# Optimization experiments

Measured on AMD Instinct MI355X. Metric: run time of the kernel, lower is better.

## Reference

```python
import jax, jax.numpy as jnp
import numpy as np

SEQ_LEN = 4096
D_MODEL = 1024
NUM_POLES = 64


def setup_inputs() -> dict:
    key = jax.random.key(0)
    k1, k2, k3 = jax.random.split(key, 3)
    z = jax.random.normal(k1, (SEQ_LEN,), dtype=jnp.float32)
    poles = jax.random.normal(k2, (D_MODEL, NUM_POLES), dtype=jnp.float32) * 0.1
    residues = jax.random.normal(k3, (D_MODEL, NUM_POLES), dtype=jnp.float32) * 0.01
    return {"z": z, "poles": poles, "residues": residues}


def reference(z, poles, residues):
    # z: (S,), poles/residues: (D, P) -> out: (S, D)
    # Cauchy sum: out[s, d] = sum_p residues[d, p] / (z[s] - poles[d, p])
    denom = z[:, None, None] - poles[None, :, :]          # (S, D, P)
    result = jnp.sum(residues[None, :, :] / denom, axis=-1)  # (S, D)
    return result
```

## Files before the change

kernel.cpp:

```cpp
#include <hip/hip_runtime.h>
#include <hip/hip_bf16.h>

#define S_TOTAL 4096
#define D_TOTAL 1024
#define NPOLES  64
#define NPAIRS  32
#define S_PER_BLOCK 32
#define BLOCK 256

__device__ __forceinline__ float sanitize_finite(float x) {
    const float lim = 1.0e38f;
    const unsigned u = __float_as_uint(x);
    if ((u & 0x7f800000u) == 0x7f800000u)
        return (u & 0x80000000u) ? -lim : lim;
    return fminf(fmaxf(x, -lim), lim);
}

__global__ __launch_bounds__(BLOCK, 2) void cauchy_pair_kernel(
    const float* __restrict__ z,
    const float* __restrict__ poles,
    const float* __restrict__ residues,
    float* __restrict__ out)
{
    const int d  = blockIdx.y * BLOCK + threadIdx.x;
    const int s0 = blockIdx.x * S_PER_BLOCK;

    float cA[NPAIRS], cB[NPAIRS], cS[NPAIRS], cP[NPAIRS];
    const float* pp = poles    + (size_t)d * NPOLES;
    const float* rr = residues + (size_t)d * NPOLES;
#pragma unroll
    for (int i = 0; i < NPOLES / 4; ++i) {
        const float4 p4 = *reinterpret_cast<const float4*>(pp + 4 * i);
        const float4 r4 = *reinterpret_cast<const float4*>(rr + 4 * i);
        const int q = 2 * i;
        cS[q + 0] = p4.x + p4.y;
        cP[q + 0] = p4.x * p4.y;
        cA[q + 0] = r4.x + r4.y;
        cB[q + 0] = -fmaf(r4.x, p4.y, r4.y * p4.x);
        cS[q + 1] = p4.z + p4.w;
        cP[q + 1] = p4.z * p4.w;
        cA[q + 1] = r4.z + r4.w;
        cB[q + 1] = -fmaf(r4.z, p4.w, r4.w * p4.z);
    }

    for (int si = 0; si < S_PER_BLOCK; si += 4) {
        const float z0 = z[s0 + si + 0];
        const float z1 = z[s0 + si + 1];
        const float z2 = z[s0 + si + 2];
        const float z3 = z[s0 + si + 3];
        float a0 = 0.f, a1 = 0.f, a2 = 0.f, a3 = 0.f;
#pragma unroll
        for (int q = 0; q < NPAIRS; ++q) {
            const float A = cA[q], B = cB[q], S = cS[q], P = cP[q];
            {   const float den = fmaf(z0, z0 - S, P);
                a0 = fmaf(fmaf(A, z0, B), __builtin_amdgcn_rcpf(den), a0); }
            {   const float den = fmaf(z1, z1 - S, P);
                a1 = fmaf(fmaf(A, z1, B), __builtin_amdgcn_rcpf(den), a1); }
            {   const float den = fmaf(z2, z2 - S, P);
                a2 = fmaf(fmaf(A, z2, B), __builtin_amdgcn_rcpf(den), a2); }
            {   const float den = fmaf(z3, z3 - S, P);
                a3 = fmaf(fmaf(A, z3, B), __builtin_amdgcn_rcpf(den), a3); }
        }
        out[(size_t)(s0 + si + 0) * D_TOTAL + d] = sanitize_finite(a0);
        out[(size_t)(s0 + si + 1) * D_TOTAL + d] = sanitize_finite(a1);
        out[(size_t)(s0 + si + 2) * D_TOTAL + d] = sanitize_finite(a2);
        out[(size_t)(s0 + si + 3) * D_TOTAL + d] = sanitize_finite(a3);
    }
}

extern "C" void kernel_launch(void* const* d_in, const int* in_sizes, int n_in,
                              void* d_out, int out_size, void* d_ws, size_t ws_size,
                              hipStream_t stream) {
    const float* z        = (const float*)d_in[0];
    const float* poles    = (const float*)d_in[1];
    const float* residues = (const float*)d_in[2];
    float* out            = (float*)d_out;

    dim3 grid(S_TOTAL / S_PER_BLOCK, D_TOTAL / BLOCK);
    dim3 block(BLOCK);
    cauchy_pair_kernel<<<grid, block, 0, stream>>>(z, poles, residues, out);
}
```

Before: 89.58 us.

## Split pole pairs across two threads per channel with shared-memory reduction

Each d channel is now handled by two threads, each owning 16 of the 32 pole pairs. Partial sums are combined through shared memory, and each half writes two of the four output rows. This halves per-thread register coefficients so occupancy can rise (launch bounds go from 2 to 4 blocks) and doubles the grid. In exchange it adds two barriers and LDS traffic per 4-row iteration, and shared loads of poles/residues now read strided halves.

```diff
diff --git a/kernel.cpp b/kernel.cpp
--- a/kernel.cpp
+++ b/kernel.cpp
@@ -4,7 +4,8 @@
 #define S_TOTAL 4096
 #define D_TOTAL 1024
 #define NPOLES  64
-#define NPAIRS  32
+#define D_PER_BLOCK 128
+#define PAIRS_PER_THREAD 16
 #define S_PER_BLOCK 32
 #define BLOCK 256
 
@@ -16,20 +17,26 @@
     return fminf(fmaxf(x, -lim), lim);
 }
 
-__global__ __launch_bounds__(BLOCK, 2) void cauchy_pair_kernel(
+__global__ __launch_bounds__(BLOCK, 4) void cauchy_split_kernel(
     const float* __restrict__ z,
     const float* __restrict__ poles,
     const float* __restrict__ residues,
     float* __restrict__ out)
 {
-    const int d  = blockIdx.y * BLOCK + threadIdx.x;
-    const int s0 = blockIdx.x * S_PER_BLOCK;
+    const int tid = threadIdx.x;
+    const int dl  = tid & (D_PER_BLOCK - 1);
+    const int h   = tid >> 7;
+    const int d   = blockIdx.y * D_PER_BLOCK + dl;
+    const int s0  = blockIdx.x * S_PER_BLOCK;
 
-    float cA[NPAIRS], cB[NPAIRS], cS[NPAIRS], cP[NPAIRS];
-    const float* pp = poles    + (size_t)d * NPOLES;
-    const float* rr = residues + (size_t)d * NPOLES;
+    __shared__ float xchg[4][2][D_PER_BLOCK];
+
+    float cA[PAIRS_PER_THREAD], cB[PAIRS_PER_THREAD],
+          cS[PAIRS_PER_THREAD], cP[PAIRS_PER_THREAD];
+    const float* pp = poles    + (size_t)d * NPOLES + h * 32;
+    const float* rr = residues + (size_t)d * NPOLES + h * 32;
 #pragma unroll
-    for (int i = 0; i < NPOLES / 4; ++i) {
+    for (int i = 0; i < 8; ++i) {
         const float4 p4 = *reinterpret_cast<const float4*>(pp + 4 * i);
         const float4 r4 = *reinterpret_cast<const float4*>(rr + 4 * i);
         const int q = 2 * i;
@@ -50,7 +57,7 @@
         const float z3 = z[s0 + si + 3];
         float a0 = 0.f, a1 = 0.f, a2 = 0.f, a3 = 0.f;
 #pragma unroll
-        for (int q = 0; q < NPAIRS; ++q) {
+        for (int q = 0; q < PAIRS_PER_THREAD; ++q) {
             const float A = cA[q], B = cB[q], S = cS[q], P = cP[q];
             {   const float den = fmaf(z0, z0 - S, P);
                 a0 = fmaf(fmaf(A, z0, B), __builtin_amdgcn_rcpf(den), a0); }
@@ -61,10 +68,22 @@
             {   const float den = fmaf(z3, z3 - S, P);
                 a3 = fmaf(fmaf(A, z3, B), __builtin_amdgcn_rcpf(den), a3); }
         }
-        out[(size_t)(s0 + si + 0) * D_TOTAL + d] = sanitize_finite(a0);
-        out[(size_t)(s0 + si + 1) * D_TOTAL + d] = sanitize_finite(a1);
-        out[(size_t)(s0 + si + 2) * D_TOTAL + d] = sanitize_finite(a2);
-        out[(size_t)(s0 + si + 3) * D_TOTAL + d] = sanitize_finite(a3);
+        xchg[0][h][dl] = a0;
+        xchg[1][h][dl] = a1;
+        xchg[2][h][dl] = a2;
+        xchg[3][h][dl] = a3;
+        __syncthreads();
+        const int oh = h ^ 1;
+        a0 += xchg[0][oh][dl];
+        a1 += xchg[1][oh][dl];
+        a2 += xchg[2][oh][dl];
+        a3 += xchg[3][oh][dl];
+        const float v0 = h ? a2 : a0;
+        const float v1 = h ? a3 : a1;
+        const int   r0 = si + 2 * h;
+        out[(size_t)(s0 + r0 + 0) * D_TOTAL + d] = sanitize_finite(v0);
+        out[(size_t)(s0 + r0 + 1) * D_TOTAL + d] = sanitize_finite(v1);
+        __syncthreads();
     }
 }
 
@@ -76,7 +95,7 @@
     const float* residues = (const float*)d_in[2];
     float* out            = (float*)d_out;
 
-    dim3 grid(S_TOTAL / S_PER_BLOCK, D_TOTAL / BLOCK);
+    dim3 grid(S_TOTAL / S_PER_BLOCK, D_TOTAL / D_PER_BLOCK);
     dim3 block(BLOCK);
-    cauchy_pair_kernel<<<grid, block, 0, stream>>>(z, poles, residues, out);
+    cauchy_split_kernel<<<grid, block, 0, stream>>>(z, poles, residues, out);
 }
```

Measured after the change: 89.50 us. Within noise of the previous version (-0.1%).
